# Optimization experiments

Hardware: AMD Instinct MI355X
Metric: run time of the kernel (lower is better)

The kernel has to match this reference:

```python
import math
import jax, jax.numpy as jnp
import numpy as np

jax.config.update("jax_enable_x64", True)

NUM_HEADS = 4
D_INNER = 256
D_STATE = 256
HEADDIM = D_INNER // NUM_HEADS
NUM_GRAPHS = 8
L_NODES = 512
N_NODES = NUM_GRAPHS * L_NODES
N_EDGES = 65536
TOL = 0.05  # self.tol


def dag_inverse(A, n):
    # Doubling Neumann series: (I+A)(I+A^2)(I+A^4)... = sum_{k<2^ceil(log2 n)} A^k
    # equals (I - A)^{-1} when A is nilpotent (DAG with diameter <= n).
    j = 2 ** math.ceil(math.log2(n))
    I = jnp.eye(A.shape[-1], dtype=A.dtype)
    last = A
    out = I + A
    for _ in range(2, int(math.log2(j)) + 1):
        last = last @ last
        out = out @ (I + last)
    return out


def _forward(x, Bmat, Cmat, dt, dt_edge, dt_bias, D, edge_index, data_batch, diameter):
    Bg, L, H, Hd = NUM_GRAPHS, L_NODES, NUM_HEADS, HEADDIM
    N = x.shape[0]
    # nodes are sorted by graph with equal graph sizes -> local index within graph
    local = jnp.arange(N) - data_batch * L

    def to_dense(v):  # (N, ...) -> (Bg, L, ...), equivalent of to_dense_batch
        return jnp.zeros((Bg, L) + v.shape[1:], v.dtype).at[data_batch, local].set(v)

    x_r = to_dense(x).reshape(Bg, L, H, Hd).transpose(0, 2, 1, 3)  # b n l h
    B_b = jnp.broadcast_to(to_dense(Bmat)[:, None], (Bg, H, L, D_STATE))  # broadcast_bc_in_heads
    C_b = jnp.broadcast_to(to_dense(Cmat)[:, None], (Bg, H, L, D_STATE))

    dt3 = dt.reshape(N, H, 4).transpose(2, 1, 0)  # 'l (n c) -> c n l'
    dt_self_d = to_dense(dt3[3].T).transpose(0, 2, 1)  # (b, n, l)

    def mul_dt_A(d):
        # A_log is a zeros buffer (with_A=False) -> A = -exp(0) = -1
        return -jax.nn.softplus(d + dt_bias[None, :, None])

    dt_A_node = mul_dt_A(dt3[:3])  # (3, n, N)
    dt_A_edge = mul_dt_A(dt_edge.reshape(-1, H, 1).transpose(2, 1, 0))  # (1, n, E)

    src, dst = edge_index[0], edge_index[1]
    dt_A = (dt_A_node[0][:, src] + dt_A_node[1][:, dst] + dt_A_edge[0]) / 3.0  # (n, E)
    vals = jnp.exp(dt_A).T  # (E, n)
    # to_dense_adj: scatter-add edge attrs into dense (b, l1, l2, n)
    adj = jnp.zeros((Bg, L, L, H), vals.dtype).at[
        data_batch[src], local[src], local[dst]].add(vals)
    adj = adj.transpose(0, 3, 1, 2)  # (b, n, l1, l2)

    dt_dummy = to_dense(jnp.exp(dt_A_node[2]).T).transpose(0, 2, 1)  # (b, n, l)
    # normalize_mat('sum_leq', sub_constraint='max')
    normalizer = jnp.maximum(1.0, adj.sum(-1) + dt_dummy)
    A_mat = adj / (normalizer[..., None] + TOL)

    # I_minus_A: fp64 doubling inverse of (I - A^T)
    Lm = dag_inverse(jnp.swapaxes(A_mat.astype(jnp.float64), -1, -2), diameter)
    Lm = Lm.astype(x.dtype)
    L_norm = Lm * dt_self_d[:, :, None, :]  # L * dt_self.unsqueeze(-2)

    y = jnp.einsum('bnld,bnlt,bntd,bnth->bnlh', C_b, L_norm, B_b, x_r)
    y = y + x_r * D[None, :, None, None]
    y = y.transpose(0, 2, 3, 1).reshape(Bg, L, Hd * H)  # 'b n l h -> b l (h n)'
    return y.reshape(N, Hd * H)  # mask is all-True (equal-size graphs)


def setup_inputs():
    key = jax.random.key(0)
    ks = jax.random.split(key, 8)
    x = jax.random.normal(ks[0], (N_NODES, D_INNER), dtype=jnp.float32)
    Bmat = jax.random.normal(ks[1], (N_NODES, D_STATE), dtype=jnp.float32)
    Cmat = jax.random.normal(ks[2], (N_NODES, D_STATE), dtype=jnp.float32)
    dt = jax.random.normal(ks[3], (N_NODES, NUM_HEADS * 4), dtype=jnp.float32)
    dt_edge = jax.random.normal(ks[4], (N_EDGES, NUM_HEADS), dtype=jnp.float32)
    per_graph = N_EDGES // NUM_GRAPHS
    g = jnp.repeat(jnp.arange(NUM_GRAPHS), per_graph)
    src = g * L_NODES + jax.random.randint(ks[5], (N_EDGES,), 0, L_NODES)
    dst = g * L_NODES + jax.random.randint(ks[6], (N_EDGES,), 0, L_NODES)
    edge_index = jnp.stack([src, dst]).astype(jnp.int32)
    data_batch = jnp.repeat(jnp.arange(NUM_GRAPHS), L_NODES).astype(jnp.int32)
    # dt_bias init as in module __init__
    dt_min, dt_max = 1e-3, 1e-1
    u = jax.random.uniform(ks[7], (NUM_HEADS,))
    dtv = jnp.exp(u * (math.log(dt_max) - math.log(dt_min)) + math.log(dt_min))
    dtv = jnp.clip(dtv, 1e-4, None)
    dt_bias = (dtv + jnp.log(-jnp.expm1(-dtv))).astype(jnp.float32)
    D = jnp.ones((NUM_HEADS,), dtype=jnp.float32)
    return {"x": x, "Bmat": Bmat, "Cmat": Cmat, "dt": dt, "dt_edge": dt_edge,
            "dt_bias": dt_bias, "D": D, "edge_index": edge_index,
            "data_batch": data_batch, "diameter": 32}


def reference(x, Bmat, Cmat, dt, dt_edge, dt_bias, D, edge_index, data_batch, diameter):
    return _forward(x, Bmat, Cmat, dt, dt_edge, dt_bias, D, edge_index, data_batch, diameter)
```

## Files before the change

kernel.cpp:

```cpp
#include <hip/hip_runtime.h>
#include <math.h>

#define N_EDGES 65536
#define LNODE 512
#define DSTATE 256
#define DINNER 256
#define HEADD 64

using bf16x8 = __attribute__((ext_vector_type(8))) short;
using f32x4  = __attribute__((ext_vector_type(4))) float;
using us4    = __attribute__((ext_vector_type(4))) unsigned short;
using us8    = __attribute__((ext_vector_type(8))) unsigned short;

__device__ __forceinline__ float softplusf(float z) {
  return (z > 0.0f) ? (z + log1pf(expf(-z))) : log1pf(expf(z));
}
__device__ __forceinline__ float bf2f(unsigned short u) {
  unsigned int x = ((unsigned int)u) << 16;
  return __builtin_bit_cast(float, x);
}
__device__ __forceinline__ unsigned short f2bf(float f) {
  unsigned int x = __builtin_bit_cast(unsigned int, f);
  x += 0x7fffu + ((x >> 16) & 1u);
  return (unsigned short)(x >> 16);
}

__global__ void scatter_edges_kernel(const float* __restrict__ dt,
                                     const float* __restrict__ dt_edge,
                                     const float* __restrict__ dt_bias,
                                     const int* __restrict__ edge_index,
                                     float* __restrict__ G,
                                     float* __restrict__ colsum) {
  int t = blockIdx.x * blockDim.x + threadIdx.x;
  if (t >= N_EDGES * 4) return;
  int e = t >> 2;
  int n = t & 3;
  int src = edge_index[e];
  int dst = edge_index[N_EDGES + e];
  float bias = dt_bias[n];
  float z0 = dt[src * 16 + n * 4 + 0] + bias;
  float z1 = dt[dst * 16 + n * 4 + 1] + bias;
  float z2 = dt_edge[e * 4 + n] + bias;
  float val = expf(-(softplusf(z0) + softplusf(z1) + softplusf(z2)) * (1.0f / 3.0f));
  int b = src >> 9;
  int l1 = src & 511;
  int l2 = dst & 511;
  int bn = b * 4 + n;
  atomicAdd(&G[(((size_t)bn) << 18) + ((size_t)l2 << 9) + l1], val);
  atomicAdd(&colsum[bn * 512 + l1], val);
}

__global__ __launch_bounds__(256) void conv_kernel(const float* __restrict__ G,
                                                   const float* __restrict__ colsum,
                                                   const float* __restrict__ dt,
                                                   const float* __restrict__ dt_bias,
                                                   unsigned short* __restrict__ Prm,
                                                   unsigned short* __restrict__ Pt,
                                                   unsigned short* __restrict__ Q) {
  const int bn = blockIdx.y;
  const int n = bn & 3, b = bn >> 2;
  const size_t base = (size_t)bn << 18;
  const int tile = blockIdx.x;
  const int ro = (tile >> 4) << 5;
  const int co = (tile & 15) << 5;
  __shared__ float lds[32][33];
  __shared__ float sinv[32];
  const int t = threadIdx.x;
  if (t < 32) {
    const int col = co + t;
    float ssum = colsum[bn * 512 + col];
    float bias = dt_bias[n];
    float dummy = expf(-softplusf(dt[(size_t)(b * 512 + col) * 16 + n * 4 + 2] + bias));
    float norm = fmaxf(1.0f, ssum + dummy);
    sinv[t] = 1.0f / (norm + 0.05f);
  }
  __syncthreads();
  const int tr = t >> 3;
  const int tc0 = (t & 7) << 2;
  float4 gv = *(const float4*)(G + base + (size_t)(ro + tr) * 512 + co + tc0);
  float vv[4] = {gv.x, gv.y, gv.z, gv.w};
  us4 p, q;
#pragma unroll
  for (int j = 0; j < 4; ++j) {
    vv[j] *= sinv[tc0 + j];
    p[j] = f2bf(vv[j]);
    float qq = vv[j] + (((ro + tr) == (co + tc0 + j)) ? 1.0f : 0.0f);
    q[j] = f2bf(qq);
    lds[tc0 + j][tr] = vv[j];
  }
  *(us4*)(Prm + base + (size_t)(ro + tr) * 512 + co + tc0) = p;
  *(us4*)(Q + base + (size_t)(ro + tr) * 512 + co + tc0) = q;
  __syncthreads();
  us4 pt;
#pragma unroll
  for (int j = 0; j < 4; ++j) pt[j] = f2bf(lds[tr][tc0 + j]);
  *(us4*)(Pt + base + (size_t)(co + tr) * 512 + ro + tc0) = pt;
}

__global__ __launch_bounds__(256) void gemm_pair_kernel(
    const unsigned short* __restrict__ A0, const unsigned short* __restrict__ B0,
    unsigned short* __restrict__ C0rm, unsigned short* __restrict__ C0t,
    const unsigned short* __restrict__ Q0,
    const unsigned short* __restrict__ A1, const unsigned short* __restrict__ B1,
    unsigned short* __restrict__ C1rm, unsigned short* __restrict__ C1t,
    const unsigned short* __restrict__ Q1) {
  const int f = (blockIdx.z * gridDim.y + blockIdx.y) * gridDim.x + blockIdx.x;
  const int rres = f & 7;
  const int q = f >> 3;
  const int tile = q & 15;
  const int kk_ = ((q >> 4) << 3) + rres;
  const int bn = kk_ & 31;
  const int z = kk_ >> 5;

  const unsigned short* A    = z ? A1 : A0;
  const unsigned short* Bt   = z ? B1 : B0;
  unsigned short* Crm        = z ? C1rm : C0rm;
  unsigned short* Ct         = z ? C1t : C0t;
  const unsigned short* Qadd = z ? Q1 : Q0;

  const size_t off = (size_t)bn << 18;
  A += off; Bt += off;
  if (Crm) Crm += off;
  if (Ct) Ct += off;
  if (Qadd) Qadd += off;
  const int m0 = (tile >> 2) << 7;
  const int n0 = (tile & 3) << 7;
  __shared__ __align__(16) char lds[65536];
  const int tid = threadIdx.x;
  const int lane = tid & 63;
  const int w = tid >> 6;
  const int wr = w >> 1, wc = w & 1;
  const int lr = lane >> 3, g = lane & 7;

  f32x4 acc[4][4];
#pragma unroll
  for (int i = 0; i < 4; ++i)
#pragma unroll
    for (int j = 0; j < 4; ++j) acc[i][j] = (f32x4)(0.0f);

  auto stage = [&](int buf, int k0) {
    char* la = lds + buf * 32768;
    char* lb = la + 16384;
#pragma unroll
    for (int s = 0; s < 4; ++s) {
      const int r = s * 32 + w * 8 + lr;
      const unsigned short* ga = A + (size_t)(m0 + r) * 512 + k0 + ((g ^ (r & 7)) << 3);
      __builtin_amdgcn_global_load_lds(
          (const __attribute__((address_space(1))) void*)ga,
          (__attribute__((address_space(3))) void*)(la + s * 4096 + w * 1024 + (lane << 4)),
          16, 0, 0);
      const unsigned short* gb = Bt + (size_t)(n0 + r) * 512 + k0 + ((g ^ (r & 7)) << 3);
      __builtin_amdgcn_global_load_lds(
          (const __attribute__((address_space(1))) void*)gb,
          (__attribute__((address_space(3))) void*)(lb + s * 4096 + w * 1024 + (lane << 4)),
          16, 0, 0);
    }
  };

  stage(0, 0);

#pragma unroll
  for (int t = 0; t < 8; ++t) {
    const int cur = t & 1;
    if (t < 7) {
      stage(cur ^ 1, (t + 1) * 64);
      asm volatile("s_waitcnt vmcnt(8)" ::: "memory");
    } else {
      asm volatile("s_waitcnt vmcnt(0)" ::: "memory");
    }
    __builtin_amdgcn_s_barrier();
    __builtin_amdgcn_sched_barrier(0);
    char* la = lds + cur * 32768;
    char* lb = la + 16384;
#pragma unroll
    for (int kk = 0; kk < 2; ++kk) {
      const int gk = kk * 4 + (lane >> 4);
      bf16x8 av[4], bv[4];
#pragma unroll
      for (int mi = 0; mi < 4; ++mi) {
        const int r = wr * 64 + mi * 16 + (lane & 15);
        av[mi] = *(const bf16x8*)(la + r * 128 + ((gk ^ (r & 7)) << 4));
      }
#pragma unroll
      for (int ni = 0; ni < 4; ++ni) {
        const int r = wc * 64 + ni * 16 + (lane & 15);
        bv[ni] = *(const bf16x8*)(lb + r * 128 + ((gk ^ (r & 7)) << 4));
      }
#pragma unroll
      for (int mi = 0; mi < 4; ++mi)
#pragma unroll
        for (int ni = 0; ni < 4; ++ni)
          acc[mi][ni] = __builtin_amdgcn_mfma_f32_16x16x32_bf16(av[mi], bv[ni], acc[mi][ni], 0, 0, 0);
    }
    __builtin_amdgcn_sched_barrier(0);
    __builtin_amdgcn_s_barrier();
  }

  const int cl = lane & 15;
  const int rg = (lane >> 4) << 2;
  unsigned short* tl = (unsigned short*)lds;
#pragma unroll
  for (int mi = 0; mi < 4; ++mi) {
#pragma unroll
    for (int ni = 0; ni < 4; ++ni) {
      const int lrow = wr * 64 + mi * 16 + rg;
      const int lcol = wc * 64 + ni * 16 + cl;
      const int gr = m0 + lrow;
      const int gc = n0 + lcol;
      float v0 = acc[mi][ni][0], v1 = acc[mi][ni][1];
      float v2 = acc[mi][ni][2], v3 = acc[mi][ni][3];
      if (Qadd) {
        v0 += bf2f(Qadd[(size_t)(gr + 0) * 512 + gc]);
        v1 += bf2f(Qadd[(size_t)(gr + 1) * 512 + gc]);
        v2 += bf2f(Qadd[(size_t)(gr + 2) * 512 + gc]);
        v3 += bf2f(Qadd[(size_t)(gr + 3) * 512 + gc]);
      }
      unsigned short h0 = f2bf(v0), h1 = f2bf(v1), h2 = f2bf(v2), h3 = f2bf(v3);
      if (Crm) {
        Crm[(size_t)(gr + 0) * 512 + gc] = h0;
        Crm[(size_t)(gr + 1) * 512 + gc] = h1;
        Crm[(size_t)(gr + 2) * 512 + gc] = h2;
        Crm[(size_t)(gr + 3) * 512 + gc] = h3;
      }
      if (Ct) {
        tl[lcol * 136 + lrow + 0] = h0;
        tl[lcol * 136 + lrow + 1] = h1;
        tl[lcol * 136 + lrow + 2] = h2;
        tl[lcol * 136 + lrow + 3] = h3;
      }
    }
  }
  if (Ct) {
    __syncthreads();
    const int c = tid >> 1;
    const int rh = (tid & 1) << 6;
    const unsigned short* srcp = tl + c * 136 + rh;
    unsigned short* dstp = Ct + (size_t)(n0 + c) * 512 + m0 + rh;
#pragma unroll
    for (int u = 0; u < 8; ++u)
      *(us8*)(dstp + u * 8) = *(const us8*)(srcp + u * 8);
  }
}

__global__ __launch_bounds__(256) void gemm_nt_kernel(const float* __restrict__ Cm,
                                                      const float* __restrict__ Bm,
                                                      float* __restrict__ S) {
  const int f = blockIdx.y * gridDim.x + blockIdx.x;
  const int b = f & 7;
  const int tile = f >> 3;
  const float* Ab = Cm + (size_t)b * LNODE * DSTATE;
  const float* Bb = Bm + (size_t)b * LNODE * DSTATE;
  float* Sb = S + ((size_t)b << 18);
  const int m0 = (tile >> 3) << 6;
  const int n0 = (tile & 7) << 6;
  __shared__ float As[16][68];
  __shared__ float Bs[16][68];
  const int tid = threadIdx.x;
  const int tx = tid & 15, ty = tid >> 4;
  const int srow = tid >> 2, skq = tid & 3;
  float acc[4][4] = {};
  for (int k0 = 0; k0 < DSTATE; k0 += 16) {
    float4 a = *(const float4*)(Ab + (size_t)(m0 + srow) * DSTATE + k0 + skq * 4);
    As[skq * 4 + 0][srow] = a.x; As[skq * 4 + 1][srow] = a.y;
    As[skq * 4 + 2][srow] = a.z; As[skq * 4 + 3][srow] = a.w;
    float4 c = *(const float4*)(Bb + (size_t)(n0 + srow) * DSTATE + k0 + skq * 4);
    Bs[skq * 4 + 0][srow] = c.x; Bs[skq * 4 + 1][srow] = c.y;
    Bs[skq * 4 + 2][srow] = c.z; Bs[skq * 4 + 3][srow] = c.w;
    __syncthreads();
#pragma unroll
    for (int k = 0; k < 16; ++k) {
      float av[4], bv[4];
      *(float4*)(av) = *(const float4*)(&As[k][ty * 4]);
      *(float4*)(bv) = *(const float4*)(&Bs[k][tx * 4]);
#pragma unroll
      for (int i = 0; i < 4; ++i)
#pragma unroll
        for (int j = 0; j < 4; ++j)
          acc[i][j] = fmaf(av[i], bv[j], acc[i][j]);
    }
    __syncthreads();
  }
#pragma unroll
  for (int i = 0; i < 4; ++i) {
    float* sp = Sb + (size_t)(m0 + ty * 4 + i) * 512 + n0 + tx * 4;
    *(float4*)sp = make_float4(acc[i][0], acc[i][1], acc[i][2], acc[i][3]);
  }
}

__global__ __launch_bounds__(256) void final_fused_kernel(
    const unsigned short* __restrict__ Lm, const float* __restrict__ S,
    const float* __restrict__ dt, const float* __restrict__ x,
    float* __restrict__ P) {
  const int f = (blockIdx.z * gridDim.y + blockIdx.y) * gridDim.x + blockIdx.x;
  const int rres = f & 7;
  const int q = f >> 3;
  const int sub = q & 15;
  const int bn = ((q >> 4) << 3) + rres;
  const int ltile = sub & 3;
  const int kg = sub >> 2;
  const int n = bn & 3, b = bn >> 2;
  const unsigned short* Lb = Lm + ((size_t)bn << 18);
  const float* Sb = S + ((size_t)b << 18);
  const float* xb = x + (size_t)b * LNODE * DINNER + n * HEADD;
  const int m0 = ltile << 7;
  const int kbase = kg << 7;
  __shared__ float Ms[16][132];
  __shared__ float Xs[16][64];
  __shared__ float dts_all[128];
  const int tid = threadIdx.x;
  const int tx = tid & 15, ty = tid >> 4;
  if (tid < 128)
    dts_all[tid] = dt[(size_t)(b * 512 + kbase + tid) * 16 + n * 4 + 3];
  __syncthreads();
  float acc[8][4] = {};
  for (int kk0 = 0; kk0 < 128; kk0 += 16) {
    const int k0 = kbase + kk0;
#pragma unroll
    for (int s = 0; s < 2; ++s) {
      int fid = tid + s * 256;
      int m = fid >> 2, kq = fid & 3;
      us4 lm = *(const us4*)(Lb + (size_t)(m0 + m) * 512 + k0 + kq * 4);
      float4 sv = *(const float4*)(Sb + (size_t)(m0 + m) * 512 + k0 + kq * 4);
      Ms[kq * 4 + 0][m] = bf2f(lm[0]) * sv.x * dts_all[kk0 + kq * 4 + 0];
      Ms[kq * 4 + 1][m] = bf2f(lm[1]) * sv.y * dts_all[kk0 + kq * 4 + 1];
      Ms[kq * 4 + 2][m] = bf2f(lm[2]) * sv.z * dts_all[kk0 + kq * 4 + 2];
      Ms[kq * 4 + 3][m] = bf2f(lm[3]) * sv.w * dts_all[kk0 + kq * 4 + 3];
    }
    {
      int kk = tid >> 4, hq = tid & 15;
      float4 v = *(const float4*)(xb + (size_t)(k0 + kk) * DINNER + hq * 4);
      *(float4*)(&Xs[kk][hq * 4]) = v;
    }
    __syncthreads();
#pragma unroll
    for (int k = 0; k < 16; ++k) {
      float mv[8], xv[4];
      *(float4*)(mv)     = *(const float4*)(&Ms[k][ty * 8]);
      *(float4*)(mv + 4) = *(const float4*)(&Ms[k][ty * 8 + 4]);
      *(float4*)(xv)     = *(const float4*)(&Xs[k][tx * 4]);
#pragma unroll
      for (int i = 0; i < 8; ++i)
#pragma unroll
        for (int j = 0; j < 4; ++j)
          acc[i][j] = fmaf(mv[i], xv[j], acc[i][j]);
    }
    __syncthreads();
  }
  float* Pb = P + (((size_t)(kg * 32 + bn)) << 15);
#pragma unroll
  for (int i = 0; i < 8; ++i) {
    const int l = m0 + ty * 8 + i;
    *(float4*)(Pb + (size_t)l * 64 + tx * 4) =
        make_float4(acc[i][0], acc[i][1], acc[i][2], acc[i][3]);
  }
}

__global__ __launch_bounds__(256) void reduce_out_kernel(
    const float* __restrict__ P, const float* __restrict__ x,
    const float* __restrict__ Dv, float* __restrict__ out) {
  int t = blockIdx.x * 256 + threadIdx.x;
  int h = t & 63;
  int l = (t >> 6) & 511;
  int b = t >> 15;
  float4 v;
#pragma unroll
  for (int n = 0; n < 4; ++n) {
    int bn = b * 4 + n;
    float s = 0.0f;
#pragma unroll
    for (int kg = 0; kg < 4; ++kg)
      s += P[(((size_t)(kg * 32 + bn)) << 15) + (size_t)l * 64 + h];
    s += x[(size_t)(b * 512 + l) * 256 + n * 64 + h] * Dv[n];
    ((float*)&v)[n] = s;
  }
  *(float4*)(out + (size_t)(b * 512 + l) * 256 + h * 4) = v;
}

extern "C" void kernel_launch(void* const* d_in, const int* in_sizes, int n_in,
                              void* d_out, int out_size, void* d_ws, size_t ws_size,
                              hipStream_t stream) {
  const float* x        = (const float*)d_in[0];
  const float* Bmat     = (const float*)d_in[1];
  const float* Cmat     = (const float*)d_in[2];
  const float* dt       = (const float*)d_in[3];
  const float* dt_edge  = (const float*)d_in[4];
  const float* dt_bias  = (const float*)d_in[5];
  const float* Dv       = (const float*)d_in[6];
  const int* edge_index = (const int*)d_in[7];
  float* out = (float*)d_out;

  char* wsb = (char*)d_ws;
  const size_t SL = 16777216;
  unsigned short* sA = (unsigned short*)(wsb + 0 * SL);
  unsigned short* sB = (unsigned short*)(wsb + 1 * SL);
  unsigned short* sC = (unsigned short*)(wsb + 2 * SL);
  unsigned short* sD = (unsigned short*)(wsb + 3 * SL);
  unsigned short* sE = (unsigned short*)(wsb + 4 * SL);
  unsigned short* sF = (unsigned short*)(wsb + 5 * SL);
  float* G      = (float*)(wsb + 3 * SL);
  float* Sbuf   = (float*)(wsb + 5 * SL);
  float* Pbuf   = (float*)(wsb + 3 * SL);
  float* colsum = (float*)(wsb + 6 * SL);

  hipMemsetAsync(G, 0, 33554432, stream);
  hipMemsetAsync(colsum, 0, 32 * 512 * 4, stream);
  scatter_edges_kernel<<<1024, 256, 0, stream>>>(dt, dt_edge, dt_bias, edge_index, G, colsum);
  conv_kernel<<<dim3(256, 32), 256, 0, stream>>>(G, colsum, dt, dt_bias, sA, sB, sC);

  dim3 g1(16, 32, 1), g2(16, 32, 2);
  gemm_pair_kernel<<<g1, 256, 0, stream>>>(sA, sB, sD, sE, nullptr,
                                           nullptr, nullptr, nullptr, nullptr, nullptr);
  gemm_pair_kernel<<<g2, 256, 0, stream>>>(sD, sE, sA, sB, nullptr,
                                           sC, sE, sF, nullptr, sC);
  gemm_pair_kernel<<<g2, 256, 0, stream>>>(sA, sB, sC, sD, nullptr,
                                           sF, sB, sE, nullptr, sF);
  gemm_nt_kernel<<<dim3(64, 8), 256, 0, stream>>>(Cmat, Bmat, Sbuf);
  gemm_pair_kernel<<<g2, 256, 0, stream>>>(sC, sD, nullptr, sA, nullptr,
                                           sE, sD, sB, nullptr, sE);
  gemm_pair_kernel<<<g1, 256, 0, stream>>>(sB, sA, sC, nullptr, sB,
                                           nullptr, nullptr, nullptr, nullptr, nullptr);

  final_fused_kernel<<<dim3(4, 4, 32), 256, 0, stream>>>(sC, Sbuf, dt, x, Pbuf);
  reduce_out_kernel<<<1024, 256, 0, stream>>>(Pbuf, x, Dv, out);
}
```

Baseline: 233.7 us.

## Replace double-buffered LDS DMA staging with register-prefetched single LDS buffer

```diff
diff --git a/kernel.cpp b/kernel.cpp
--- a/kernel.cpp
+++ b/kernel.cpp
@@ -97,7 +97,7 @@
   *(us4*)(Pt + base + (size_t)(co + tr) * 512 + ro + tc0) = pt;
 }
 
-__global__ __launch_bounds__(256) void gemm_pair_kernel(
+__global__ __launch_bounds__(256, 3) void gemm_pair_kernel(
     const unsigned short* __restrict__ A0, const unsigned short* __restrict__ B0,
     unsigned short* __restrict__ C0rm, unsigned short* __restrict__ C0t,
     const unsigned short* __restrict__ Q0,
@@ -125,7 +125,9 @@
   if (Qadd) Qadd += off;
   const int m0 = (tile >> 2) << 7;
   const int n0 = (tile & 3) << 7;
-  __shared__ __align__(16) char lds[65536];
+  __shared__ __align__(16) char lds[36864];
+  char* la = lds;
+  char* lb = lds + 16384;
   const int tid = threadIdx.x;
   const int lane = tid & 63;
   const int w = tid >> 6;
@@ -138,40 +140,36 @@
 #pragma unroll
     for (int j = 0; j < 4; ++j) acc[i][j] = (f32x4)(0.0f);
 
-  auto stage = [&](int buf, int k0) {
-    char* la = lds + buf * 32768;
-    char* lb = la + 16384;
+  float4 sa[4], sb[4];
+
+  auto LOADR = [&](int k0) {
 #pragma unroll
     for (int s = 0; s < 4; ++s) {
       const int r = s * 32 + w * 8 + lr;
-      const unsigned short* ga = A + (size_t)(m0 + r) * 512 + k0 + ((g ^ (r & 7)) << 3);
-      __builtin_amdgcn_global_load_lds(
-          (const __attribute__((address_space(1))) void*)ga,
-          (__attribute__((address_space(3))) void*)(la + s * 4096 + w * 1024 + (lane << 4)),
-          16, 0, 0);
-      const unsigned short* gb = Bt + (size_t)(n0 + r) * 512 + k0 + ((g ^ (r & 7)) << 3);
-      __builtin_amdgcn_global_load_lds(
-          (const __attribute__((address_space(1))) void*)gb,
-          (__attribute__((address_space(3))) void*)(lb + s * 4096 + w * 1024 + (lane << 4)),
-          16, 0, 0);
+      sa[s] = *(const float4*)(A + (size_t)(m0 + r) * 512 + k0 + g * 8);
+      sb[s] = *(const float4*)(Bt + (size_t)(n0 + r) * 512 + k0 + g * 8);
     }
   };
-
-  stage(0, 0);
+  auto WRITELDS = [&]() {
+#pragma unroll
+    for (int s = 0; s < 4; ++s) {
+      const int r = s * 32 + w * 8 + lr;
+      const int o = r * 128 + ((g ^ (r & 7)) << 4);
+      *(float4*)(la + o) = sa[s];
+      *(float4*)(lb + o) = sb[s];
+    }
+  };
+
+  LOADR(0);
+  WRITELDS();
+  asm volatile("s_waitcnt lgkmcnt(0)" ::: "memory");
+  __builtin_amdgcn_sched_barrier(0);
+  __builtin_amdgcn_s_barrier();
+  __builtin_amdgcn_sched_barrier(0);
 
 #pragma unroll
   for (int t = 0; t < 8; ++t) {
-    const int cur = t & 1;
-    if (t < 7) {
-      stage(cur ^ 1, (t + 1) * 64);
-      asm volatile("s_waitcnt vmcnt(8)" ::: "memory");
-    } else {
-      asm volatile("s_waitcnt vmcnt(0)" ::: "memory");
-    }
-    __builtin_amdgcn_s_barrier();
-    __builtin_amdgcn_sched_barrier(0);
-    char* la = lds + cur * 32768;
-    char* lb = la + 16384;
+    if (t < 7) LOADR((t + 1) * 64);
 #pragma unroll
     for (int kk = 0; kk < 2; ++kk) {
       const int gk = kk * 4 + (lane >> 4);
@@ -194,6 +192,14 @@
     }
     __builtin_amdgcn_sched_barrier(0);
     __builtin_amdgcn_s_barrier();
+    __builtin_amdgcn_sched_barrier(0);
+    if (t < 7) {
+      WRITELDS();
+      asm volatile("s_waitcnt lgkmcnt(0)" ::: "memory");
+      __builtin_amdgcn_sched_barrier(0);
+      __builtin_amdgcn_s_barrier();
+      __builtin_amdgcn_sched_barrier(0);
+    }
   }
 
   const int cl = lane & 15;
@@ -223,10 +229,10 @@
         Crm[(size_t)(gr + 3) * 512 + gc] = h3;
       }
       if (Ct) {
-        tl[lcol * 136 + lrow + 0] = h0;
-        tl[lcol * 136 + lrow + 1] = h1;
-        tl[lcol * 136 + lrow + 2] = h2;
-        tl[lcol * 136 + lrow + 3] = h3;
+        tl[lcol * 132 + lrow + 0] = h0;
+        tl[lcol * 132 + lrow + 1] = h1;
+        tl[lcol * 132 + lrow + 2] = h2;
+        tl[lcol * 132 + lrow + 3] = h3;
       }
     }
   }
@@ -234,7 +240,7 @@
     __syncthreads();
     const int c = tid >> 1;
     const int rh = (tid & 1) << 6;
-    const unsigned short* srcp = tl + c * 136 + rh;
+    const unsigned short* srcp = tl + c * 132 + rh;
     unsigned short* dstp = Ct + (size_t)(n0 + c) * 512 + m0 + rh;
 #pragma unroll
     for (int u = 0; u < 8; ++u)
```

Measured after the change: 444.8 us. 1.9x slower.
